# Optimization experiments

Measured on AMD Instinct MI355X. Metric: run time of the kernel, lower is better.

The kernel has to match this reference:

```python
import jax, jax.numpy as jnp
import numpy as np

N, E, F, O = 50000, 800000, 128, 128
LOW = [0, 1, 2, 4]           # single-radius (low-pass) channels
BAND = [(0, 1), (1, 2), (2, 4)]  # two-radius (band-pass) channels
KMAX = 4


def setup_inputs() -> dict:
    key = jax.random.key(0)
    ks = jax.random.split(key, 16)
    x = jax.random.normal(ks[0], (N, F), dtype=jnp.float32)
    # edges with no self-loops (dst = src + offset mod N, offset in [1, N))
    src = jax.random.randint(ks[1], (E,), 0, N)
    off = jax.random.randint(ks[2], (E,), 1, N)
    dst = (src + off) % N
    edge_index = jnp.stack([src, dst]).astype(jnp.int64)
    s_lin = 1.0 / np.sqrt(F)
    s_att = 1.0 / np.sqrt(O)
    W_low = jax.random.normal(ks[3], (len(LOW), F, O), jnp.float32) * s_lin
    b_low = jnp.zeros((len(LOW), O), jnp.float32)
    W_band = jax.random.normal(ks[4], (len(BAND), F, O), jnp.float32) * s_lin
    b_band = jnp.zeros((len(BAND), O), jnp.float32)
    att_pre_low = jax.random.normal(ks[5], (1, O), jnp.float32) * s_att
    att_channel_low = jax.random.normal(ks[6], (1, O), jnp.float32) * s_att
    att_pre_band = jax.random.normal(ks[7], (1, O), jnp.float32) * s_att
    att_channel_band = jax.random.normal(ks[8], (1, O), jnp.float32) * s_att
    W_mlp = jax.random.normal(ks[9], (2 * O, O), jnp.float32) * (1.0 / np.sqrt(2 * O))
    b_mlp = jnp.zeros((O,), jnp.float32)
    return {"x": x, "edge_index": edge_index, "W_low": W_low, "b_low": b_low,
            "W_band": W_band, "b_band": b_band,
            "att_pre_low": att_pre_low, "att_channel_low": att_channel_low,
            "att_pre_band": att_pre_band, "att_channel_band": att_channel_band,
            "W_mlp": W_mlp, "b_mlp": b_mlp}


def _sym_norm_weights(src, dst, n, dtype):
    # degree over edges WITHOUT self-loops; self-loop weight is 1, all / 2
    deg = jax.ops.segment_sum(jnp.ones(src.shape[0], dtype), dst, num_segments=n)
    d_inv_sqrt = jnp.where(deg > 0, 1.0 / jnp.sqrt(jnp.maximum(deg, 1e-12)), 0.0)
    return d_inv_sqrt[src] * d_inv_sqrt[dst] * 0.5  # [E]; self-loop coeff is 0.5


def _propagate(x, src, dst, w, n):
    # out[i] = sum_{e: dst=i} w_e * x[src_e] + 0.5 * x[i]  (self-loop term)
    msg = x[src] * w[:, None]  # [E, O]
    return jax.ops.segment_sum(msg, dst, num_segments=n) + 0.5 * x


def _att_combine(h, att_pre, att_ch):
    # h: [C, N, O]; single head attention over channels
    a = jax.nn.relu(h)
    h_pre = a.mean(axis=0)  # [N, O]
    logits = jax.nn.relu(h_pre @ att_pre[0] + jnp.einsum('cno,o->cn', a, att_ch[0]))
    alpha = jax.nn.softmax(logits, axis=0)  # softmax over channels
    return jnp.einsum('cn,cno->no', alpha, h)


def reference(x, edge_index, W_low, b_low, W_band, b_band,
              att_pre_low, att_channel_low, att_pre_band, att_channel_band,
              W_mlp, b_mlp):
    src, dst = edge_index[0], edge_index[1]
    n = x.shape[0]
    w = _sym_norm_weights(src, dst, n, x.dtype)
    # K-hop propagation, store aggregates at required radii
    aggs = {0: x}
    a = x
    for k in range(1, KMAX + 1):
        a = _propagate(a, src, dst, w, n)
        aggs[k] = a
    feats_low = jnp.stack([aggs[k] for k in LOW])                     # [Cl, N, F]
    feats_band = jnp.stack([aggs[k1] - aggs[k2] for k1, k2 in BAND])  # [Cb, N, F]
    h_low = jnp.einsum('cnf,cfo->cno', feats_low, W_low) + b_low[:, None, :]
    h_band = jnp.einsum('cnf,cfo->cno', feats_band, W_band) + b_band[:, None, :]
    out_low = _att_combine(h_low, att_pre_low, att_channel_low)
    out_band = _att_combine(h_band, att_pre_band, att_channel_band)
    out = jnp.concatenate([out_low, out_band], axis=-1) @ W_mlp + b_mlp
    return out
```

## Files before the change

kernel.cpp:

```cpp
#include <hip/hip_runtime.h>
#include <math.h>

#define NN 50000
#define NE 800000
#define TM 16

typedef _Float16 half4v __attribute__((ext_vector_type(4)));
typedef _Float16 half8v __attribute__((ext_vector_type(8)));
typedef float f32x4 __attribute__((ext_vector_type(4)));

__device__ __forceinline__ float relu(float v) { return fmaxf(v, 0.0f); }

__global__ __launch_bounds__(256) void k_deg(const int* __restrict__ ei,
                                             int* __restrict__ deg) {
  int e = blockIdx.x * 256 + threadIdx.x;
  if (e < NE) atomicAdd(&deg[ei[NE + e]], 1);
}

__global__ __launch_bounds__(256) void k_dinv(const int* __restrict__ deg,
                                              float* __restrict__ dinv) {
  int i = blockIdx.x * 256 + threadIdx.x;
  if (i < NN) {
    int d = deg[i];
    dinv[i] = d > 0 ? 1.0f / sqrtf((float)d) : 0.0f;
  }
}

__global__ __launch_bounds__(1024) void k_scan(const int* __restrict__ deg,
                                               int* __restrict__ rowptr) {
  __shared__ int swave[16];
  __shared__ int scarry;
  const int tid = threadIdx.x;
  const int lane = tid & 63;
  const int wid = tid >> 6;
  if (tid == 0) scarry = 0;
  __syncthreads();
  for (int base = 0; base < NN; base += 1024) {
    int i = base + tid;
    int v = (i < NN) ? deg[i] : 0;
    int sum = v;
#pragma unroll
    for (int off = 1; off < 64; off <<= 1) {
      int t = __shfl_up(sum, off);
      if (lane >= off) sum += t;
    }
    if (lane == 63) swave[wid] = sum;
    __syncthreads();
    int wbase = 0;
    for (int w = 0; w < wid; ++w) wbase += swave[w];
    int carry = scarry;
    if (i < NN) rowptr[i] = carry + wbase + sum - v;
    __syncthreads();
    if (tid == 1023) scarry = carry + wbase + sum;
    __syncthreads();
  }
  if (tid == 0) rowptr[NN] = scarry;
}

__global__ __launch_bounds__(256) void k_fill(const int* __restrict__ ei,
                                              const float* __restrict__ dinv,
                                              const int* __restrict__ rowptr,
                                              int* __restrict__ fill,
                                              int* __restrict__ col,
                                              float* __restrict__ wgt) {
  int e = blockIdx.x * 256 + threadIdx.x;
  if (e < NE) {
    int s = ei[e];
    int d = ei[NE + e];
    float w = dinv[s] * dinv[d] * 0.5f;
    int pos = rowptr[d] + atomicAdd(&fill[d], 1);
    col[pos] = s;
    wgt[pos] = w;
  }
}

__global__ __launch_bounds__(256) void k_x2h(const float* __restrict__ x,
                                             _Float16* __restrict__ xh) {
  int i = blockIdx.x * 256 + threadIdx.x;
  if (i < NN * 32) {
    float4 v = ((const float4*)x)[i];
    half4v h;
    h[0] = (_Float16)v.x; h[1] = (_Float16)v.y;
    h[2] = (_Float16)v.z; h[3] = (_Float16)v.w;
    ((half4v*)xh)[i] = h;
  }
}

__global__ __launch_bounds__(256) void k_hop16(const _Float16* __restrict__ in,
                                               _Float16* __restrict__ out,
                                               const int* __restrict__ rowptr,
                                               const int* __restrict__ col,
                                               const float* __restrict__ wgt) {
  int g = (blockIdx.x * 256 + threadIdx.x) >> 4;
  int lane = threadIdx.x & 15;
  if (g >= NN) return;
  const half8v* in8 = (const half8v*)in;
  half8v a = in8[(size_t)g * 16 + lane];
  float acc[8];
#pragma unroll
  for (int j = 0; j < 8; ++j) acc[j] = 0.5f * (float)a[j];
  int e = rowptr[g], e1 = rowptr[g + 1];
  for (; e + 4 <= e1; e += 4) {
    int c0 = col[e], c1 = col[e + 1], c2 = col[e + 2], c3 = col[e + 3];
    float w0 = wgt[e], w1 = wgt[e + 1], w2 = wgt[e + 2], w3 = wgt[e + 3];
    half8v v0 = in8[(size_t)c0 * 16 + lane];
    half8v v1 = in8[(size_t)c1 * 16 + lane];
    half8v v2 = in8[(size_t)c2 * 16 + lane];
    half8v v3 = in8[(size_t)c3 * 16 + lane];
#pragma unroll
    for (int j = 0; j < 8; ++j)
      acc[j] += w0 * (float)v0[j] + w1 * (float)v1[j] +
                w2 * (float)v2[j] + w3 * (float)v3[j];
  }
  for (; e < e1; ++e) {
    float w = wgt[e];
    half8v v = in8[(size_t)col[e] * 16 + lane];
#pragma unroll
    for (int j = 0; j < 8; ++j) acc[j] += w * (float)v[j];
  }
  half8v r;
#pragma unroll
  for (int j = 0; j < 8; ++j) r[j] = (_Float16)acc[j];
  ((half8v*)out)[(size_t)g * 16 + lane] = r;
}

__global__ __launch_bounds__(256) void k_prep(const float* __restrict__ W_low,
                                              const float* __restrict__ W_band,
                                              const float* __restrict__ W_mlp,
                                              _Float16* __restrict__ WTs) {
  int m = blockIdx.x;
  const float* src;
  if (m < 4)      src = W_low + m * 16384;
  else if (m < 7) src = W_band + (m - 4) * 16384;
  else            src = W_mlp + (m - 7) * 16384;
  _Float16* dst = WTs + (size_t)m * 16384;
  for (int s = threadIdx.x; s < 2048; s += 256) {
    int ct = s >> 8;
    int ks = (s >> 6) & 3;
    int lane = s & 63;
    int mcol = lane & 15, kg = lane >> 4;
    int colc = ct * 16 + mcol;
    int k0 = ks * 32 + 4 * kg;
    _Float16* d = dst + (size_t)s * 8;
#pragma unroll
    for (int j = 0; j < 4; ++j) d[j] = (_Float16)src[(k0 + j) * 128 + colc];
#pragma unroll
    for (int j = 0; j < 4; ++j) d[4 + j] = (_Float16)src[(k0 + 16 + j) * 128 + colc];
  }
}

__global__ __launch_bounds__(256, 3) void k_fused(
    const _Float16* __restrict__ xh, const _Float16* __restrict__ a1,
    const _Float16* __restrict__ a2, const _Float16* __restrict__ a4,
    const _Float16* __restrict__ WTs,
    const float* __restrict__ b_low, const float* __restrict__ b_band,
    const float* __restrict__ apre_l, const float* __restrict__ ach_l,
    const float* __restrict__ apre_b, const float* __restrict__ ach_b,
    const float* __restrict__ b_mlp, float* __restrict__ out) {
  __shared__ _Float16 sH[7][TM][136];
  __shared__ _Float16 sV[TM][264];

  const int tid = threadIdx.x;
  const int wid = tid >> 6;
  const int lane = tid & 63;
  const int mrow = lane & 15;
  const int kg = lane >> 4;
  const int node0 = blockIdx.x * TM;
  const int colw = wid * 32;

  half8v base[4][4];
  {
    const _Float16* arrs[4] = {xh, a1, a2, a4};
#pragma unroll
    for (int t = 0; t < 4; ++t) {
      const _Float16* p = arrs[t] + (size_t)(node0 + mrow) * 128;
#pragma unroll
      for (int ks = 0; ks < 4; ++ks) {
        half4v lo = *(const half4v*)&p[ks * 32 + 4 * kg];
        half4v hi = *(const half4v*)&p[ks * 32 + 4 * kg + 16];
        base[t][ks] = __builtin_shufflevector(lo, hi, 0, 1, 2, 3, 4, 5, 6, 7);
      }
    }
  }

#pragma unroll
  for (int c = 0; c < 7; ++c) {
    const int ia = (c < 4) ? c : (c - 4);
    const int ib = (c < 4) ? -1 : (c - 3);
    const _Float16* wc = WTs + (size_t)c * 16384;
    f32x4 acc0 = {0.f, 0.f, 0.f, 0.f}, acc1 = {0.f, 0.f, 0.f, 0.f};
#pragma unroll
    for (int ks = 0; ks < 4; ++ks) {
      half8v af = (ib < 0) ? base[ia][ks] : (base[ia][ks] - base[ib][ks]);
      half8v bf0 = *(const half8v*)&wc[(size_t)(2 * wid) * 2048 + ks * 512 + lane * 8];
      half8v bf1 = *(const half8v*)&wc[(size_t)(2 * wid + 1) * 2048 + ks * 512 + lane * 8];
      acc0 = __builtin_amdgcn_mfma_f32_16x16x32_f16(af, bf0, acc0, 0, 0, 0);
      acc1 = __builtin_amdgcn_mfma_f32_16x16x32_f16(af, bf1, acc1, 0, 0, 0);
    }
    const float* bias = (c < 4) ? (b_low + c * 128) : (b_band + (c - 4) * 128);
    float bv0 = bias[colw + mrow];
    float bv1 = bias[colw + 16 + mrow];
#pragma unroll
    for (int r = 0; r < 4; ++r) {
      sH[c][4 * kg + r][colw + mrow] = (_Float16)(acc0[r] + bv0);
      sH[c][4 * kg + r][colw + 16 + mrow] = (_Float16)(acc1[r] + bv1);
    }
  }
  __syncthreads();

  {
    const int n = tid >> 4;
    const int cb = (tid & 15) * 8;
    float apl[8], acl[8], apb[8], acb[8];
#pragma unroll
    for (int j = 0; j < 8; ++j) {
      apl[j] = apre_l[cb + j]; acl[j] = ach_l[cb + j];
      apb[j] = apre_b[cb + j]; acb[j] = ach_b[cb + j];
    }
    float dpl = 0.f, dpb = 0.f;
    float sarr[7];
#pragma unroll
    for (int c = 0; c < 7; ++c) {
      float sp = 0.f, sc = 0.f;
#pragma unroll
      for (int j = 0; j < 8; ++j) {
        float h = (float)sH[c][n][cb + j];
        float r = relu(h);
        if (c < 4) { sp += r * apl[j]; sc += r * acl[j]; }
        else       { sp += r * apb[j]; sc += r * acb[j]; }
      }
      if (c < 4) dpl += sp; else dpb += sp;
      sarr[c] = sc;
    }
    dpl *= 0.25f;
    dpb *= (1.0f / 3.0f);
#pragma unroll
    for (int m = 1; m <= 8; m <<= 1) {
      dpl += __shfl_xor(dpl, m);
      dpb += __shfl_xor(dpb, m);
#pragma unroll
      for (int c = 0; c < 7; ++c) sarr[c] += __shfl_xor(sarr[c], m);
    }
    float lg[7];
#pragma unroll
    for (int c = 0; c < 7; ++c)
      lg[c] = relu((c < 4 ? dpl : dpb) + sarr[c]);
    float ml = fmaxf(fmaxf(lg[0], lg[1]), fmaxf(lg[2], lg[3]));
    float e0 = expf(lg[0] - ml), e1 = expf(lg[1] - ml);
    float e2 = expf(lg[2] - ml), e3 = expf(lg[3] - ml);
    float invl = 1.0f / (e0 + e1 + e2 + e3);
    float mb = fmaxf(fmaxf(lg[4], lg[5]), lg[6]);
    float f4 = expf(lg[4] - mb), f5 = expf(lg[5] - mb), f6 = expf(lg[6] - mb);
    float invb = 1.0f / (f4 + f5 + f6);
    float al[7];
    al[0] = e0 * invl; al[1] = e1 * invl; al[2] = e2 * invl; al[3] = e3 * invl;
    al[4] = f4 * invb; al[5] = f5 * invb; al[6] = f6 * invb;
    half8v vl8, vb8;
#pragma unroll
    for (int j = 0; j < 8; ++j) {
      float vl = 0.f, vb = 0.f;
#pragma unroll
      for (int c = 0; c < 4; ++c) vl += al[c] * (float)sH[c][n][cb + j];
#pragma unroll
      for (int c = 4; c < 7; ++c) vb += al[c] * (float)sH[c][n][cb + j];
      vl8[j] = (_Float16)vl;
      vb8[j] = (_Float16)vb;
    }
    *(half8v*)&sV[n][cb] = vl8;
    *(half8v*)&sV[n][128 + cb] = vb8;
  }
  __syncthreads();

  f32x4 m0 = {0.f, 0.f, 0.f, 0.f}, m1 = {0.f, 0.f, 0.f, 0.f};
#pragma unroll
  for (int hh = 0; hh < 2; ++hh) {
    const _Float16* wm = WTs + (size_t)(7 + hh) * 16384;
#pragma unroll
    for (int ks = 0; ks < 4; ++ks) {
      int ka = hh * 128 + ks * 32 + 4 * kg;
      half4v aa = *(const half4v*)&sV[mrow][ka];
      half4v ab = *(const half4v*)&sV[mrow][ka + 16];
      half8v af = __builtin_shufflevector(aa, ab, 0, 1, 2, 3, 4, 5, 6, 7);
      half8v bf0 = *(const half8v*)&wm[(size_t)(2 * wid) * 2048 + ks * 512 + lane * 8];
      half8v bf1 = *(const half8v*)&wm[(size_t)(2 * wid + 1) * 2048 + ks * 512 + lane * 8];
      m0 = __builtin_amdgcn_mfma_f32_16x16x32_f16(af, bf0, m0, 0, 0, 0);
      m1 = __builtin_amdgcn_mfma_f32_16x16x32_f16(af, bf1, m1, 0, 0, 0);
    }
  }
  float bm0 = b_mlp[colw + mrow];
  float bm1 = b_mlp[colw + 16 + mrow];
#pragma unroll
  for (int r = 0; r < 4; ++r) {
    out[(size_t)(node0 + 4 * kg + r) * 128 + colw + mrow] = m0[r] + bm0;
    out[(size_t)(node0 + 4 * kg + r) * 128 + colw + 16 + mrow] = m1[r] + bm1;
  }
}

extern "C" void kernel_launch(void* const* d_in, const int* in_sizes, int n_in,
                              void* d_out, int out_size, void* d_ws, size_t ws_size,
                              hipStream_t stream) {
  const float* x      = (const float*)d_in[0];
  const int* ei       = (const int*)d_in[1];
  const float* W_low  = (const float*)d_in[2];
  const float* b_low  = (const float*)d_in[3];
  const float* W_band = (const float*)d_in[4];
  const float* b_band = (const float*)d_in[5];
  const float* apre_l = (const float*)d_in[6];
  const float* ach_l  = (const float*)d_in[7];
  const float* apre_b = (const float*)d_in[8];
  const float* ach_b  = (const float*)d_in[9];
  const float* W_mlp  = (const float*)d_in[10];
  const float* b_mlp  = (const float*)d_in[11];
  float* out = (float*)d_out;

  char* ws = (char*)d_ws;
  size_t off = 0;
  auto take = [&](size_t bytes) -> void* {
    void* p = ws + off;
    off = (off + bytes + 255) & ~(size_t)255;
    return p;
  };
  int*   deg    = (int*)take((size_t)NN * 4);
  int*   fill   = (int*)take((size_t)NN * 4);
  size_t zero_bytes = off;
  float* dinv   = (float*)take((size_t)NN * 4);
  int*   rowptr = (int*)take((size_t)(NN + 1) * 4);
  int*   col    = (int*)take((size_t)NE * 4);
  float* wgt    = (float*)take((size_t)NE * 4);
  _Float16* xh  = (_Float16*)take((size_t)NN * 128 * 2);
  _Float16* a1h = (_Float16*)take((size_t)NN * 128 * 2);
  _Float16* a2h = (_Float16*)take((size_t)NN * 128 * 2);
  _Float16* a3h = (_Float16*)take((size_t)NN * 128 * 2);
  _Float16* a4h = (_Float16*)take((size_t)NN * 128 * 2);
  _Float16* WTs = (_Float16*)take((size_t)9 * 16384 * 2);
  (void)ws_size; (void)in_sizes; (void)n_in; (void)out_size;

  hipMemsetAsync(d_ws, 0, zero_bytes, stream);
  k_prep<<<9, 256, 0, stream>>>(W_low, W_band, W_mlp, WTs);
  k_x2h<<<(NN * 32 + 255) / 256, 256, 0, stream>>>(x, xh);
  k_deg<<<(NE + 255) / 256, 256, 0, stream>>>(ei, deg);
  k_dinv<<<(NN + 255) / 256, 256, 0, stream>>>(deg, dinv);
  k_scan<<<1, 1024, 0, stream>>>(deg, rowptr);
  k_fill<<<(NE + 255) / 256, 256, 0, stream>>>(ei, dinv, rowptr, fill, col, wgt);
  k_hop16<<<(NN * 16 + 255) / 256, 256, 0, stream>>>(xh,  a1h, rowptr, col, wgt);
  k_hop16<<<(NN * 16 + 255) / 256, 256, 0, stream>>>(a1h, a2h, rowptr, col, wgt);
  k_hop16<<<(NN * 16 + 255) / 256, 256, 0, stream>>>(a2h, a3h, rowptr, col, wgt);
  k_hop16<<<(NN * 16 + 255) / 256, 256, 0, stream>>>(a3h, a4h, rowptr, col, wgt);
  k_fused<<<NN / TM, 256, 0, stream>>>(xh, a1h, a2h, a4h, WTs, b_low, b_band,
                                       apre_l, ach_l, apre_b, ach_b, b_mlp, out);
}
```

Measured before the change: 371.2 us.

## Split hop feature columns across XCDs to localize gathered slices in L2

The propagation kernel now gives each block one quarter of the 128 feature columns for 64 nodes, and maps block IDs so that each pair of XCDs handles the same column slice. Each XCD's L2 then only holds a 32-column slice of the gathered feature matrix, which is meant to raise cache hit rates for the random neighbor gathers. In exchange, the row pointer, column and weight arrays are read four times, and each gather is only 64 bytes per node per slice. It also relies on round-robin block-to-XCD dispatch, which is a hardware scheduling assumption.

```diff
diff --git a/kernel.cpp b/kernel.cpp
--- a/kernel.cpp
+++ b/kernel.cpp
@@ -86,27 +86,35 @@
   }
 }
 
-__global__ __launch_bounds__(256) void k_hop16(const _Float16* __restrict__ in,
+__global__ __launch_bounds__(256) void k_hop_s(const _Float16* __restrict__ in,
                                                _Float16* __restrict__ out,
                                                const int* __restrict__ rowptr,
                                                const int* __restrict__ col,
                                                const float* __restrict__ wgt) {
-  int g = (blockIdx.x * 256 + threadIdx.x) >> 4;
-  int lane = threadIdx.x & 15;
-  if (g >= NN) return;
+  const int bid = blockIdx.x;
+  const int xcd = bid & 7;
+  const int s = xcd >> 1;
+  const int halfp = xcd & 1;
+  const int nb = (bid >> 3) * 2 + halfp;
+  const int t = threadIdx.x;
+  const int node = nb * 64 + (t >> 2);
+  const int lane = t & 3;
+  if (node >= NN) return;
   const half8v* in8 = (const half8v*)in;
-  half8v a = in8[(size_t)g * 16 + lane];
+  const int coff = s * 4 + lane;
+  const size_t self = (size_t)node * 16 + coff;
+  half8v a = in8[self];
   float acc[8];
 #pragma unroll
   for (int j = 0; j < 8; ++j) acc[j] = 0.5f * (float)a[j];
-  int e = rowptr[g], e1 = rowptr[g + 1];
+  int e = rowptr[node], e1 = rowptr[node + 1];
   for (; e + 4 <= e1; e += 4) {
     int c0 = col[e], c1 = col[e + 1], c2 = col[e + 2], c3 = col[e + 3];
     float w0 = wgt[e], w1 = wgt[e + 1], w2 = wgt[e + 2], w3 = wgt[e + 3];
-    half8v v0 = in8[(size_t)c0 * 16 + lane];
-    half8v v1 = in8[(size_t)c1 * 16 + lane];
-    half8v v2 = in8[(size_t)c2 * 16 + lane];
-    half8v v3 = in8[(size_t)c3 * 16 + lane];
+    half8v v0 = in8[(size_t)c0 * 16 + coff];
+    half8v v1 = in8[(size_t)c1 * 16 + coff];
+    half8v v2 = in8[(size_t)c2 * 16 + coff];
+    half8v v3 = in8[(size_t)c3 * 16 + coff];
 #pragma unroll
     for (int j = 0; j < 8; ++j)
       acc[j] += w0 * (float)v0[j] + w1 * (float)v1[j] +
@@ -114,14 +122,14 @@
   }
   for (; e < e1; ++e) {
     float w = wgt[e];
-    half8v v = in8[(size_t)col[e] * 16 + lane];
+    half8v v = in8[(size_t)col[e] * 16 + coff];
 #pragma unroll
     for (int j = 0; j < 8; ++j) acc[j] += w * (float)v[j];
   }
   half8v r;
 #pragma unroll
   for (int j = 0; j < 8; ++j) r[j] = (_Float16)acc[j];
-  ((half8v*)out)[(size_t)g * 16 + lane] = r;
+  ((half8v*)out)[self] = r;
 }
 
 __global__ __launch_bounds__(256) void k_prep(const float* __restrict__ W_low,
@@ -342,10 +350,11 @@
   k_dinv<<<(NN + 255) / 256, 256, 0, stream>>>(deg, dinv);
   k_scan<<<1, 1024, 0, stream>>>(deg, rowptr);
   k_fill<<<(NE + 255) / 256, 256, 0, stream>>>(ei, dinv, rowptr, fill, col, wgt);
-  k_hop16<<<(NN * 16 + 255) / 256, 256, 0, stream>>>(xh,  a1h, rowptr, col, wgt);
-  k_hop16<<<(NN * 16 + 255) / 256, 256, 0, stream>>>(a1h, a2h, rowptr, col, wgt);
-  k_hop16<<<(NN * 16 + 255) / 256, 256, 0, stream>>>(a2h, a3h, rowptr, col, wgt);
-  k_hop16<<<(NN * 16 + 255) / 256, 256, 0, stream>>>(a3h, a4h, rowptr, col, wgt);
+  const int hop_grid = 391 * 8;
+  k_hop_s<<<hop_grid, 256, 0, stream>>>(xh,  a1h, rowptr, col, wgt);
+  k_hop_s<<<hop_grid, 256, 0, stream>>>(a1h, a2h, rowptr, col, wgt);
+  k_hop_s<<<hop_grid, 256, 0, stream>>>(a2h, a3h, rowptr, col, wgt);
+  k_hop_s<<<hop_grid, 256, 0, stream>>>(a3h, a4h, rowptr, col, wgt);
   k_fused<<<NN / TM, 256, 0, stream>>>(xh, a1h, a2h, a4h, WTs, b_low, b_band,
                                        apre_l, ach_l, apre_b, ach_b, b_mlp, out);
 }
```

Result: slower. 454.5 us (+22.4%).

## Keep channel GEMM outputs in registers and compute attention logits from accumulators

Applied to the files above, without the earlier changes.

Drops the fp16 shared-memory staging of all seven channel outputs (sH). Attention dot products are now computed straight from the MFMA accumulators, reduced with cross-lane shuffles and a small shared-memory partial array, and the combine step uses the accumulators too. Input feature loads are interleaved with the channel GEMMs using two rolling fragment buffers instead of holding all four, and launch bounds go from 3 to 4 blocks per SM. This cuts LDS use and traffic and keeps channel outputs in fp32, at the cost of two extra syncs and 56 accumulator floats per thread of register pressure.

```diff
diff --git a/kernel.cpp b/kernel.cpp
--- a/kernel.cpp
+++ b/kernel.cpp
@@ -149,7 +149,36 @@
   }
 }
 
-__global__ __launch_bounds__(256, 3) void k_fused(
+#define LOADF(dst, src)                                                        \
+  {                                                                            \
+    const _Float16* p_ = (src) + (size_t)(node0 + mrow) * 128;                 \
+    _Pragma("unroll")                                                          \
+    for (int ks = 0; ks < 4; ++ks) {                                           \
+      half4v lo_ = *(const half4v*)&p_[ks * 32 + 4 * kg];                      \
+      half4v hi_ = *(const half4v*)&p_[ks * 32 + 4 * kg + 16];                 \
+      dst[ks] = __builtin_shufflevector(lo_, hi_, 0, 1, 2, 3, 4, 5, 6, 7);     \
+    }                                                                          \
+  }
+
+#define CH_GEMM(c, AEXPR, BIASPTR)                                             \
+  {                                                                            \
+    const _Float16* wc_ = WTs + (size_t)(c) * 16384;                           \
+    f32x4 A0_ = {0.f, 0.f, 0.f, 0.f}, A1_ = {0.f, 0.f, 0.f, 0.f};              \
+    _Pragma("unroll")                                                          \
+    for (int ks = 0; ks < 4; ++ks) {                                           \
+      half8v af_ = (AEXPR);                                                    \
+      half8v bf0_ = *(const half8v*)&wc_[(size_t)(2 * wid) * 2048 + ks * 512 + lane * 8];     \
+      half8v bf1_ = *(const half8v*)&wc_[(size_t)(2 * wid + 1) * 2048 + ks * 512 + lane * 8]; \
+      A0_ = __builtin_amdgcn_mfma_f32_16x16x32_f16(af_, bf0_, A0_, 0, 0, 0);   \
+      A1_ = __builtin_amdgcn_mfma_f32_16x16x32_f16(af_, bf1_, A1_, 0, 0, 0);   \
+    }                                                                          \
+    float bv0_ = (BIASPTR)[colw + mrow], bv1_ = (BIASPTR)[colw + 16 + mrow];   \
+    _Pragma("unroll")                                                          \
+    for (int r = 0; r < 4; ++r) { A0_[r] += bv0_; A1_[r] += bv1_; }            \
+    h0[c] = A0_; h1[c] = A1_;                                                  \
+  }
+
+__global__ __launch_bounds__(256, 4) void k_fused(
     const _Float16* __restrict__ xh, const _Float16* __restrict__ a1,
     const _Float16* __restrict__ a2, const _Float16* __restrict__ a4,
     const _Float16* __restrict__ WTs,
@@ -157,7 +186,9 @@
     const float* __restrict__ apre_l, const float* __restrict__ ach_l,
     const float* __restrict__ apre_b, const float* __restrict__ ach_b,
     const float* __restrict__ b_mlp, float* __restrict__ out) {
-  __shared__ _Float16 sH[7][TM][136];
+  __shared__ float pD[2][TM][4];
+  __shared__ float pS[7][TM][4];
+  __shared__ float aB[TM][8];
   __shared__ _Float16 sV[TM][264];
 
   const int tid = threadIdx.x;
@@ -168,83 +199,78 @@
   const int node0 = blockIdx.x * TM;
   const int colw = wid * 32;
 
-  half8v base[4][4];
-  {
-    const _Float16* arrs[4] = {xh, a1, a2, a4};
-#pragma unroll
-    for (int t = 0; t < 4; ++t) {
-      const _Float16* p = arrs[t] + (size_t)(node0 + mrow) * 128;
-#pragma unroll
-      for (int ks = 0; ks < 4; ++ks) {
-        half4v lo = *(const half4v*)&p[ks * 32 + 4 * kg];
-        half4v hi = *(const half4v*)&p[ks * 32 + 4 * kg + 16];
-        base[t][ks] = __builtin_shufflevector(lo, hi, 0, 1, 2, 3, 4, 5, 6, 7);
+  f32x4 h0[7], h1[7];
+  half8v fA[4], fB[4];
+
+  LOADF(fA, xh);
+  CH_GEMM(0, fA[ks], b_low + 0 * 128);
+  LOADF(fB, a1);
+  CH_GEMM(4, fA[ks] - fB[ks], b_band + 0 * 128);
+  CH_GEMM(1, fB[ks], b_low + 1 * 128);
+  LOADF(fA, a2);
+  CH_GEMM(5, fB[ks] - fA[ks], b_band + 1 * 128);
+  CH_GEMM(2, fA[ks], b_low + 2 * 128);
+  LOADF(fB, a4);
+  CH_GEMM(6, fA[ks] - fB[ks], b_band + 2 * 128);
+  CH_GEMM(3, fB[ks], b_low + 3 * 128);
+
+  const float apl0 = apre_l[colw + mrow], apl1 = apre_l[colw + 16 + mrow];
+  const float acl0 = ach_l[colw + mrow],  acl1 = ach_l[colw + 16 + mrow];
+  const float apb0 = apre_b[colw + mrow], apb1 = apre_b[colw + 16 + mrow];
+  const float acb0 = ach_b[colw + mrow],  acb1 = ach_b[colw + 16 + mrow];
+
+  float dpl[4] = {0.f, 0.f, 0.f, 0.f}, dpb[4] = {0.f, 0.f, 0.f, 0.f};
+  float sc[7][4];
+#pragma unroll
+  for (int c = 0; c < 7; ++c) {
+#pragma unroll
+    for (int r = 0; r < 4; ++r) {
+      float r0 = relu(h0[c][r]);
+      float r1 = relu(h1[c][r]);
+      if (c < 4) {
+        dpl[r] += r0 * apl0 + r1 * apl1;
+        sc[c][r] = r0 * acl0 + r1 * acl1;
+      } else {
+        dpb[r] += r0 * apb0 + r1 * apb1;
+        sc[c][r] = r0 * acb0 + r1 * acb1;
       }
     }
   }
-
-#pragma unroll
-  for (int c = 0; c < 7; ++c) {
-    const int ia = (c < 4) ? c : (c - 4);
-    const int ib = (c < 4) ? -1 : (c - 3);
-    const _Float16* wc = WTs + (size_t)c * 16384;
-    f32x4 acc0 = {0.f, 0.f, 0.f, 0.f}, acc1 = {0.f, 0.f, 0.f, 0.f};
-#pragma unroll
-    for (int ks = 0; ks < 4; ++ks) {
-      half8v af = (ib < 0) ? base[ia][ks] : (base[ia][ks] - base[ib][ks]);
-      half8v bf0 = *(const half8v*)&wc[(size_t)(2 * wid) * 2048 + ks * 512 + lane * 8];
-      half8v bf1 = *(const half8v*)&wc[(size_t)(2 * wid + 1) * 2048 + ks * 512 + lane * 8];
-      acc0 = __builtin_amdgcn_mfma_f32_16x16x32_f16(af, bf0, acc0, 0, 0, 0);
-      acc1 = __builtin_amdgcn_mfma_f32_16x16x32_f16(af, bf1, acc1, 0, 0, 0);
-    }
-    const float* bias = (c < 4) ? (b_low + c * 128) : (b_band + (c - 4) * 128);
-    float bv0 = bias[colw + mrow];
-    float bv1 = bias[colw + 16 + mrow];
+#pragma unroll
+  for (int r = 0; r < 4; ++r) { dpl[r] *= 0.25f; dpb[r] *= (1.0f / 3.0f); }
+#pragma unroll
+  for (int m = 1; m <= 8; m <<= 1) {
 #pragma unroll
     for (int r = 0; r < 4; ++r) {
-      sH[c][4 * kg + r][colw + mrow] = (_Float16)(acc0[r] + bv0);
-      sH[c][4 * kg + r][colw + 16 + mrow] = (_Float16)(acc1[r] + bv1);
+      dpl[r] += __shfl_xor(dpl[r], m);
+      dpb[r] += __shfl_xor(dpb[r], m);
+    }
+#pragma unroll
+    for (int c = 0; c < 7; ++c)
+#pragma unroll
+      for (int r = 0; r < 4; ++r) sc[c][r] += __shfl_xor(sc[c][r], m);
+  }
+  if (mrow == 0) {
+#pragma unroll
+    for (int r = 0; r < 4; ++r) {
+      pD[0][4 * kg + r][wid] = dpl[r];
+      pD[1][4 * kg + r][wid] = dpb[r];
+#pragma unroll
+      for (int c = 0; c < 7; ++c) pS[c][4 * kg + r][wid] = sc[c][r];
     }
   }
   __syncthreads();
 
-  {
-    const int n = tid >> 4;
-    const int cb = (tid & 15) * 8;
-    float apl[8], acl[8], apb[8], acb[8];
-#pragma unroll
-    for (int j = 0; j < 8; ++j) {
-      apl[j] = apre_l[cb + j]; acl[j] = ach_l[cb + j];
-      apb[j] = apre_b[cb + j]; acb[j] = ach_b[cb + j];
-    }
-    float dpl = 0.f, dpb = 0.f;
-    float sarr[7];
+  if (tid < TM) {
+    const int n = tid;
+    float dl = pD[0][n][0] + pD[0][n][1] + pD[0][n][2] + pD[0][n][3];
+    float db = pD[1][n][0] + pD[1][n][1] + pD[1][n][2] + pD[1][n][3];
+    float lg[7];
 #pragma unroll
     for (int c = 0; c < 7; ++c) {
-      float sp = 0.f, sc = 0.f;
-#pragma unroll
-      for (int j = 0; j < 8; ++j) {
-        float h = (float)sH[c][n][cb + j];
-        float r = relu(h);
-        if (c < 4) { sp += r * apl[j]; sc += r * acl[j]; }
-        else       { sp += r * apb[j]; sc += r * acb[j]; }
-      }
-      if (c < 4) dpl += sp; else dpb += sp;
-      sarr[c] = sc;
-    }
-    dpl *= 0.25f;
-    dpb *= (1.0f / 3.0f);
-#pragma unroll
-    for (int m = 1; m <= 8; m <<= 1) {
-      dpl += __shfl_xor(dpl, m);
-      dpb += __shfl_xor(dpb, m);
-#pragma unroll
-      for (int c = 0; c < 7; ++c) sarr[c] += __shfl_xor(sarr[c], m);
-    }
-    float lg[7];
-#pragma unroll
-    for (int c = 0; c < 7; ++c)
-      lg[c] = relu((c < 4 ? dpl : dpb) + sarr[c]);
+      float s = pS[c][n][0] + pS[c][n][1] + pS[c][n][2] + pS[c][n][3];
+      lg[c] = relu((c < 4 ? dl : db) + s);
+    }
     float ml = fmaxf(fmaxf(lg[0], lg[1]), fmaxf(lg[2], lg[3]));
     float e0 = expf(lg[0] - ml), e1 = expf(lg[1] - ml);
     float e2 = expf(lg[2] - ml), e3 = expf(lg[3] - ml);
@@ -252,22 +278,32 @@
     float mb = fmaxf(fmaxf(lg[4], lg[5]), lg[6]);
     float f4 = expf(lg[4] - mb), f5 = expf(lg[5] - mb), f6 = expf(lg[6] - mb);
     float invb = 1.0f / (f4 + f5 + f6);
-    float al[7];
-    al[0] = e0 * invl; al[1] = e1 * invl; al[2] = e2 * invl; al[3] = e3 * invl;
-    al[4] = f4 * invb; al[5] = f5 * invb; al[6] = f6 * invb;
-    half8v vl8, vb8;
-#pragma unroll
-    for (int j = 0; j < 8; ++j) {
-      float vl = 0.f, vb = 0.f;
-#pragma unroll
-      for (int c = 0; c < 4; ++c) vl += al[c] * (float)sH[c][n][cb + j];
-#pragma unroll
-      for (int c = 4; c < 7; ++c) vb += al[c] * (float)sH[c][n][cb + j];
-      vl8[j] = (_Float16)vl;
-      vb8[j] = (_Float16)vb;
-    }
-    *(half8v*)&sV[n][cb] = vl8;
-    *(half8v*)&sV[n][128 + cb] = vb8;
+    aB[n][0] = e0 * invl; aB[n][1] = e1 * invl;
+    aB[n][2] = e2 * invl; aB[n][3] = e3 * invl;
+    aB[n][4] = f4 * invb; aB[n][5] = f5 * invb; aB[n][6] = f6 * invb;
+  }
+  __syncthreads();
+
+#pragma unroll
+  for (int r = 0; r < 4; ++r) {
+    const int n = 4 * kg + r;
+    float vl0 = 0.f, vl1 = 0.f, vb0 = 0.f, vb1 = 0.f;
+#pragma unroll
+    for (int c = 0; c < 4; ++c) {
+      float a = aB[n][c];
+      vl0 += a * h0[c][r];
+      vl1 += a * h1[c][r];
+    }
+#pragma unroll
+    for (int c = 4; c < 7; ++c) {
+      float a = aB[n][c];
+      vb0 += a * h0[c][r];
+      vb1 += a * h1[c][r];
+    }
+    sV[n][colw + mrow] = (_Float16)vl0;
+    sV[n][colw + 16 + mrow] = (_Float16)vl1;
+    sV[n][128 + colw + mrow] = (_Float16)vb0;
+    sV[n][128 + colw + 16 + mrow] = (_Float16)vb1;
   }
   __syncthreads();
 
```

Result: slower. 388.9 us (+4.8%).

## Bucket CSR edges by source-node panel to improve gather locality

Applied to the files above, without the earlier changes.

Edges for each destination are split into four buckets by source-node range (panels of 12500 nodes), and the CSR is built over dst*4+panel, so each hop walks the neighbours panel by panel. The aim is to make the gathers of concurrently running groups hit a smaller region of the feature array at a time and improve L2/MALL reuse. In exchange the single-block scan now covers four times as many entries, the degree and fill arrays grow, and each node does four short loops with more tail iterations.

```diff
diff --git a/kernel.cpp b/kernel.cpp
--- a/kernel.cpp
+++ b/kernel.cpp
@@ -4,6 +4,8 @@
 #define NN 50000
 #define NE 800000
 #define TM 16
+#define NPAN 4
+#define PSZ 12500
 
 typedef _Float16 half4v __attribute__((ext_vector_type(4)));
 typedef _Float16 half8v __attribute__((ext_vector_type(8)));
@@ -11,33 +13,39 @@
 
 __device__ __forceinline__ float relu(float v) { return fmaxf(v, 0.0f); }
 
-__global__ __launch_bounds__(256) void k_deg(const int* __restrict__ ei,
-                                             int* __restrict__ deg) {
+__global__ __launch_bounds__(256) void k_deg2(const int* __restrict__ ei,
+                                              int* __restrict__ deg2) {
   int e = blockIdx.x * 256 + threadIdx.x;
-  if (e < NE) atomicAdd(&deg[ei[NE + e]], 1);
-}
-
-__global__ __launch_bounds__(256) void k_dinv(const int* __restrict__ deg,
+  if (e < NE) {
+    int s = ei[e];
+    int d = ei[NE + e];
+    atomicAdd(&deg2[d * NPAN + s / PSZ], 1);
+  }
+}
+
+__global__ __launch_bounds__(256) void k_dinv(const int* __restrict__ deg2,
                                               float* __restrict__ dinv) {
   int i = blockIdx.x * 256 + threadIdx.x;
   if (i < NN) {
-    int d = deg[i];
+    int d = deg2[i * NPAN] + deg2[i * NPAN + 1] + deg2[i * NPAN + 2] +
+            deg2[i * NPAN + 3];
     dinv[i] = d > 0 ? 1.0f / sqrtf((float)d) : 0.0f;
   }
 }
 
-__global__ __launch_bounds__(1024) void k_scan(const int* __restrict__ deg,
-                                               int* __restrict__ rowptr) {
+__global__ __launch_bounds__(1024) void k_scan(const int* __restrict__ deg2,
+                                               int* __restrict__ rowptr2) {
   __shared__ int swave[16];
   __shared__ int scarry;
   const int tid = threadIdx.x;
   const int lane = tid & 63;
   const int wid = tid >> 6;
+  const int NT = NN * NPAN;
   if (tid == 0) scarry = 0;
   __syncthreads();
-  for (int base = 0; base < NN; base += 1024) {
+  for (int base = 0; base < NT; base += 1024) {
     int i = base + tid;
-    int v = (i < NN) ? deg[i] : 0;
+    int v = (i < NT) ? deg2[i] : 0;
     int sum = v;
 #pragma unroll
     for (int off = 1; off < 64; off <<= 1) {
@@ -49,18 +57,18 @@
     int wbase = 0;
     for (int w = 0; w < wid; ++w) wbase += swave[w];
     int carry = scarry;
-    if (i < NN) rowptr[i] = carry + wbase + sum - v;
+    if (i < NT) rowptr2[i] = carry + wbase + sum - v;
     __syncthreads();
     if (tid == 1023) scarry = carry + wbase + sum;
     __syncthreads();
   }
-  if (tid == 0) rowptr[NN] = scarry;
+  if (tid == 0) rowptr2[NT] = scarry;
 }
 
 __global__ __launch_bounds__(256) void k_fill(const int* __restrict__ ei,
                                               const float* __restrict__ dinv,
-                                              const int* __restrict__ rowptr,
-                                              int* __restrict__ fill,
+                                              const int* __restrict__ rowptr2,
+                                              int* __restrict__ fill2,
                                               int* __restrict__ col,
                                               float* __restrict__ wgt) {
   int e = blockIdx.x * 256 + threadIdx.x;
@@ -68,7 +76,8 @@
     int s = ei[e];
     int d = ei[NE + e];
     float w = dinv[s] * dinv[d] * 0.5f;
-    int pos = rowptr[d] + atomicAdd(&fill[d], 1);
+    int b = d * NPAN + s / PSZ;
+    int pos = rowptr2[b] + atomicAdd(&fill2[b], 1);
     col[pos] = s;
     wgt[pos] = w;
   }
@@ -88,7 +97,7 @@
 
 __global__ __launch_bounds__(256) void k_hop16(const _Float16* __restrict__ in,
                                                _Float16* __restrict__ out,
-                                               const int* __restrict__ rowptr,
+                                               const int* __restrict__ rowptr2,
                                                const int* __restrict__ col,
                                                const float* __restrict__ wgt) {
   int g = (blockIdx.x * 256 + threadIdx.x) >> 4;
@@ -99,24 +108,28 @@
   float acc[8];
 #pragma unroll
   for (int j = 0; j < 8; ++j) acc[j] = 0.5f * (float)a[j];
-  int e = rowptr[g], e1 = rowptr[g + 1];
-  for (; e + 4 <= e1; e += 4) {
-    int c0 = col[e], c1 = col[e + 1], c2 = col[e + 2], c3 = col[e + 3];
-    float w0 = wgt[e], w1 = wgt[e + 1], w2 = wgt[e + 2], w3 = wgt[e + 3];
-    half8v v0 = in8[(size_t)c0 * 16 + lane];
-    half8v v1 = in8[(size_t)c1 * 16 + lane];
-    half8v v2 = in8[(size_t)c2 * 16 + lane];
-    half8v v3 = in8[(size_t)c3 * 16 + lane];
-#pragma unroll
-    for (int j = 0; j < 8; ++j)
-      acc[j] += w0 * (float)v0[j] + w1 * (float)v1[j] +
-                w2 * (float)v2[j] + w3 * (float)v3[j];
-  }
-  for (; e < e1; ++e) {
-    float w = wgt[e];
-    half8v v = in8[(size_t)col[e] * 16 + lane];
-#pragma unroll
-    for (int j = 0; j < 8; ++j) acc[j] += w * (float)v[j];
+#pragma unroll
+  for (int p = 0; p < NPAN; ++p) {
+    int e = rowptr2[g * NPAN + p];
+    int e1 = rowptr2[g * NPAN + p + 1];
+    for (; e + 4 <= e1; e += 4) {
+      int c0 = col[e], c1 = col[e + 1], c2 = col[e + 2], c3 = col[e + 3];
+      float w0 = wgt[e], w1 = wgt[e + 1], w2 = wgt[e + 2], w3 = wgt[e + 3];
+      half8v v0 = in8[(size_t)c0 * 16 + lane];
+      half8v v1 = in8[(size_t)c1 * 16 + lane];
+      half8v v2 = in8[(size_t)c2 * 16 + lane];
+      half8v v3 = in8[(size_t)c3 * 16 + lane];
+#pragma unroll
+      for (int j = 0; j < 8; ++j)
+        acc[j] += w0 * (float)v0[j] + w1 * (float)v1[j] +
+                  w2 * (float)v2[j] + w3 * (float)v3[j];
+    }
+    for (; e < e1; ++e) {
+      float w = wgt[e];
+      half8v v = in8[(size_t)col[e] * 16 + lane];
+#pragma unroll
+      for (int j = 0; j < 8; ++j) acc[j] += w * (float)v[j];
+    }
   }
   half8v r;
 #pragma unroll
@@ -320,11 +333,11 @@
     off = (off + bytes + 255) & ~(size_t)255;
     return p;
   };
-  int*   deg    = (int*)take((size_t)NN * 4);
-  int*   fill   = (int*)take((size_t)NN * 4);
+  int*   deg2   = (int*)take((size_t)NN * NPAN * 4);
+  int*   fill2  = (int*)take((size_t)NN * NPAN * 4);
   size_t zero_bytes = off;
   float* dinv   = (float*)take((size_t)NN * 4);
-  int*   rowptr = (int*)take((size_t)(NN + 1) * 4);
+  int*   rowptr2 = (int*)take((size_t)(NN * NPAN + 1) * 4);
   int*   col    = (int*)take((size_t)NE * 4);
   float* wgt    = (float*)take((size_t)NE * 4);
   _Float16* xh  = (_Float16*)take((size_t)NN * 128 * 2);
@@ -338,14 +351,14 @@
   hipMemsetAsync(d_ws, 0, zero_bytes, stream);
   k_prep<<<9, 256, 0, stream>>>(W_low, W_band, W_mlp, WTs);
   k_x2h<<<(NN * 32 + 255) / 256, 256, 0, stream>>>(x, xh);
-  k_deg<<<(NE + 255) / 256, 256, 0, stream>>>(ei, deg);
-  k_dinv<<<(NN + 255) / 256, 256, 0, stream>>>(deg, dinv);
-  k_scan<<<1, 1024, 0, stream>>>(deg, rowptr);
-  k_fill<<<(NE + 255) / 256, 256, 0, stream>>>(ei, dinv, rowptr, fill, col, wgt);
-  k_hop16<<<(NN * 16 + 255) / 256, 256, 0, stream>>>(xh,  a1h, rowptr, col, wgt);
-  k_hop16<<<(NN * 16 + 255) / 256, 256, 0, stream>>>(a1h, a2h, rowptr, col, wgt);
-  k_hop16<<<(NN * 16 + 255) / 256, 256, 0, stream>>>(a2h, a3h, rowptr, col, wgt);
-  k_hop16<<<(NN * 16 + 255) / 256, 256, 0, stream>>>(a3h, a4h, rowptr, col, wgt);
+  k_deg2<<<(NE + 255) / 256, 256, 0, stream>>>(ei, deg2);
+  k_dinv<<<(NN + 255) / 256, 256, 0, stream>>>(deg2, dinv);
+  k_scan<<<1, 1024, 0, stream>>>(deg2, rowptr2);
+  k_fill<<<(NE + 255) / 256, 256, 0, stream>>>(ei, dinv, rowptr2, fill2, col, wgt);
+  k_hop16<<<(NN * 16 + 255) / 256, 256, 0, stream>>>(xh,  a1h, rowptr2, col, wgt);
+  k_hop16<<<(NN * 16 + 255) / 256, 256, 0, stream>>>(a1h, a2h, rowptr2, col, wgt);
+  k_hop16<<<(NN * 16 + 255) / 256, 256, 0, stream>>>(a2h, a3h, rowptr2, col, wgt);
+  k_hop16<<<(NN * 16 + 255) / 256, 256, 0, stream>>>(a3h, a4h, rowptr2, col, wgt);
   k_fused<<<NN / TM, 256, 0, stream>>>(xh, a1h, a2h, a4h, WTs, b_low, b_band,
                                        apre_l, ach_l, apre_b, ach_b, b_mlp, out);
 }
```

Result: slower. 528.8 us (+42.5%).
